# Performance work log

Measured on AMD Instinct MI355X. Metric: run time of the kernel, lower is better.

The kernel has to match this reference:

```python
import jax, jax.numpy as jnp
import numpy as np

D = 1024       # embedding_dim
H = 16         # num_attention_heads
B = 2
S = 2048       # seq_len == context_len


def setup_inputs() -> dict:
    key = jax.random.key(0)
    k1, k2, k3 = jax.random.split(key, 3)
    X = jax.random.normal(k1, (B, S, D), dtype=jnp.float32)
    W_qkv = jax.random.normal(k2, (D, 3 * D), dtype=jnp.float32) * 0.02
    b_qkv = jnp.zeros((3 * D,), dtype=jnp.float32)
    W_out = jax.random.normal(k3, (D, D), dtype=jnp.float32) * 0.02
    b_out = jnp.zeros((D,), dtype=jnp.float32)
    return {"X": X, "W_qkv": W_qkv, "b_qkv": b_qkv, "W_out": W_out, "b_out": b_out}


def reference(X, W_qkv, b_qkv, W_out, b_out):
    b, s, d = X.shape
    hd = d // H
    # fused QKV projection (GPT-2 Conv1D == x @ W + b)
    qkv = X @ W_qkv + b_qkv                       # [b, s, 3d]
    q, k, v = jnp.split(qkv, 3, axis=2)
    # [b, h, s, hd]
    q = q.reshape(b, s, H, hd).transpose(0, 2, 1, 3)
    k = k.reshape(b, s, H, hd).transpose(0, 2, 1, 3)
    v = v.reshape(b, s, H, hd).transpose(0, 2, 1, 3)
    # NOTE: source scales by rsqrt(embedding_dim), not head_dim
    scale = 1.0 / jnp.sqrt(jnp.float32(d))
    scores = jnp.einsum("bhqd,bhkd->bhqk", q, k) * scale
    causal = jnp.tril(jnp.ones((s, s), dtype=bool))
    scores = jnp.where(causal[None, None], scores, -jnp.inf)
    # attention_dropout applied pre-softmax in source; identity at eval (p used here = 0)
    probs = jax.nn.softmax(scores, axis=-1)
    attn = jnp.einsum("bhqk,bhkd->bhqd", probs, v)
    attn = attn.transpose(0, 2, 1, 3).reshape(b, s, d)
    out = attn @ W_out + b_out                    # outwards proj; dropout eval = identity
    return out
```

## Files before the change

### kernel.cpp

```cpp
#include <hip/hip_runtime.h>

#define S_LEN 2048
#define DIM   1024
#define NHEAD 16
#define HDIM  64
#define Q_PRESCALE 0.045084220027780106f

typedef __attribute__((ext_vector_type(8))) short  short8;
typedef __attribute__((ext_vector_type(4))) float  floatx4;
typedef __attribute__((ext_vector_type(4))) unsigned short ushort4v;

__device__ inline unsigned short f2bf(float f) {
  unsigned v = __builtin_bit_cast(unsigned, f);
  v += 0x7FFFu + ((v >> 16) & 1u);
  return (unsigned short)(v >> 16);
}

__device__ inline void async16(const unsigned short* g, unsigned short* l) {
  __builtin_amdgcn_global_load_lds(
      (const __attribute__((address_space(1))) unsigned int*)g,
      (__attribute__((address_space(3))) unsigned int*)l, 16, 0, 0);
}

__global__ __launch_bounds__(256) void prep_kernel(
    const float* __restrict__ X, const float* __restrict__ Wqkv,
    const float* __restrict__ Wout, unsigned short* __restrict__ Xb,
    unsigned short* __restrict__ Wqkvt, unsigned short* __restrict__ Woutt) {
  const int j = blockIdx.x, t = threadIdx.x;
  if (j >= 4096) {
    int i = ((j - 4096) * 256 + t) * 8;
    float4 a = *(const float4*)&X[i];
    float4 b = *(const float4*)&X[i + 4];
    short8 o;
    o[0] = (short)f2bf(a.x); o[1] = (short)f2bf(a.y);
    o[2] = (short)f2bf(a.z); o[3] = (short)f2bf(a.w);
    o[4] = (short)f2bf(b.x); o[5] = (short)f2bf(b.y);
    o[6] = (short)f2bf(b.z); o[7] = (short)f2bf(b.w);
    *(short8*)&Xb[i] = o;
    return;
  }
  __shared__ unsigned short tile[32][33];
  const float* in; unsigned short* out; int N, tn, tk;
  if (j < 3072) { in = Wqkv; out = Wqkvt; N = 3072; tn = j % 96; tk = j / 96; }
  else { int u = j - 3072; in = Wout; out = Woutt; N = 1024; tn = u & 31; tk = u >> 5; }
  const int n0 = tn * 32, k0 = tk * 32;
  const int tx = t & 31, ty = t >> 5;
#pragma unroll
  for (int i = 0; i < 32; i += 8)
    tile[ty + i][tx] = f2bf(in[(size_t)(k0 + ty + i) * N + n0 + tx]);
  __syncthreads();
#pragma unroll
  for (int i = 0; i < 32; i += 8)
    out[(size_t)(n0 + ty + i) * 1024 + k0 + tx] = tile[tx][ty + i];
}

#define GEMM128_BODY(APTR, BPTR)                                                   \
  __shared__ __align__(16) unsigned short As[128][64];                             \
  __shared__ __align__(16) unsigned short Bs[128][64];                             \
  const int m0 = blockIdx.y * 128, n0 = blockIdx.x * 128;                          \
  const int t = threadIdx.x, lane = t & 63, wave = t >> 6;                         \
  const int quad = lane >> 4, l16 = lane & 15;                                     \
  const int wm = (wave >> 1) * 64, wn = (wave & 1) * 64;                           \
  const int lr = lane >> 3, lc = lane & 7, sc8 = (lc ^ lr) * 8;                    \
  const int sw = l16 & 7;                                                          \
  const int pA0 = (quad ^ sw) * 8, pA1 = ((4 + quad) ^ sw) * 8;                    \
  floatx4 acc[4][4];                                                               \
  _Pragma("unroll") for (int mi = 0; mi < 4; mi++)                                 \
      _Pragma("unroll") for (int ni = 0; ni < 4; ni++)                             \
          acc[mi][ni] = (floatx4){0.f, 0.f, 0.f, 0.f};                             \
  for (int k0 = 0; k0 < DIM; k0 += 64) {                                           \
    _Pragma("unroll") for (int i = 0; i < 4; i++) {                                \
      int rb = wave * 32 + i * 8;                                                  \
      async16(&APTR[(size_t)(m0 + rb + lr) * DIM + k0 + sc8], &As[rb][0]);         \
      async16(&BPTR[(size_t)(n0 + rb + lr) * DIM + k0 + sc8], &Bs[rb][0]);         \
    }                                                                              \
    __syncthreads();                                                               \
    short8 a0[4], a1[4];                                                           \
    _Pragma("unroll") for (int mi = 0; mi < 4; mi++) {                             \
      int row = wm + mi * 16 + l16;                                                \
      a0[mi] = *(const short8*)&As[row][pA0];                                      \
      a1[mi] = *(const short8*)&As[row][pA1];                                      \
    }                                                                              \
    _Pragma("unroll") for (int ni = 0; ni < 4; ni++) {                             \
      int row = wn + ni * 16 + l16;                                                \
      short8 b0 = *(const short8*)&Bs[row][pA0];                                   \
      short8 b1 = *(const short8*)&Bs[row][pA1];                                   \
      _Pragma("unroll") for (int mi = 0; mi < 4; mi++) {                           \
        acc[mi][ni] = __builtin_amdgcn_mfma_f32_16x16x32_bf16(a0[mi], b0, acc[mi][ni], 0, 0, 0); \
        acc[mi][ni] = __builtin_amdgcn_mfma_f32_16x16x32_bf16(a1[mi], b1, acc[mi][ni], 0, 0, 0); \
      }                                                                            \
    }                                                                              \
    __syncthreads();                                                               \
  }

__global__ __launch_bounds__(256) void gemm_qkv128(
    const unsigned short* __restrict__ Xb,
    const unsigned short* __restrict__ Wt,
    const float* __restrict__ bias,
    unsigned short* __restrict__ Qg,
    unsigned short* __restrict__ Kg,
    unsigned short* __restrict__ Vgt) {
  GEMM128_BODY(Xb, Wt)
  const int section = n0 >> 10;
  const int head = ((n0 + wn) >> 6) & 15;
#pragma unroll
  for (int mi = 0; mi < 4; mi++) {
    int mg = m0 + wm + mi * 16 + quad * 4;
    int bb = mg >> 11, sb = mg & 2047;
    size_t y = (size_t)bb * NHEAD + head;
    if (section == 2) {
#pragma unroll
      for (int ni = 0; ni < 4; ni++) {
        int hdi = ni * 16 + l16;
        float bv = bias[n0 + wn + hdi];
        ushort4v o;
#pragma unroll
        for (int r = 0; r < 4; r++) o[r] = f2bf(acc[mi][ni][r] + bv);
        *(ushort4v*)&Vgt[(y * HDIM + hdi) * S_LEN + sb] = o;
      }
    } else if (section == 0) {
#pragma unroll
      for (int ni = 0; ni < 4; ni++) {
        int hdi = ni * 16 + l16;
        float bv = bias[n0 + wn + hdi];
#pragma unroll
        for (int r = 0; r < 4; r++)
          Qg[(y * S_LEN + sb + r) * HDIM + hdi] = f2bf((acc[mi][ni][r] + bv) * Q_PRESCALE);
      }
    } else {
#pragma unroll
      for (int ni = 0; ni < 4; ni++) {
        int hdi = ni * 16 + l16;
        float bv = bias[n0 + wn + hdi];
#pragma unroll
        for (int r = 0; r < 4; r++)
          Kg[(y * S_LEN + sb + r) * HDIM + hdi] = f2bf(acc[mi][ni][r] + bv);
      }
    }
  }
}

__global__ __launch_bounds__(256) void gemm_out128(
    const unsigned short* __restrict__ A,
    const unsigned short* __restrict__ Wt,
    const float* __restrict__ bias,
    float* __restrict__ outp) {
  GEMM128_BODY(A, Wt)
#pragma unroll
  for (int ni = 0; ni < 4; ni++) {
    int n = n0 + wn + ni * 16 + l16;
    float bv = bias[n];
#pragma unroll
    for (int mi = 0; mi < 4; mi++) {
      int mg = m0 + wm + mi * 16 + quad * 4;
#pragma unroll
      for (int r = 0; r < 4; r++)
        outp[(size_t)(mg + r) * DIM + n] = acc[mi][ni][r] + bv;
    }
  }
}

__global__ __launch_bounds__(256) void gemm_qkv_kernel(
    const float* __restrict__ X,
    const unsigned short* __restrict__ Wt,
    const float* __restrict__ bias,
    unsigned short* __restrict__ Qg,
    unsigned short* __restrict__ Kg,
    unsigned short* __restrict__ Vgt,
    int g0, int G) {
  __shared__ __align__(16) unsigned short As[64][72];
  __shared__ __align__(16) unsigned short Bs[64][72];
  const int tn = blockIdx.x;
  const int section = tn / G, within = tn % G;
  const int n0 = section * 1024 + (g0 + within) * 64;
  const int m0 = blockIdx.y * 64;
  const int t = threadIdx.x, lane = t & 63, wave = t >> 6;
  const int quad = lane >> 4, l16 = lane & 15;

  floatx4 acc[4];
#pragma unroll
  for (int i = 0; i < 4; i++) acc[i] = (floatx4){0.f, 0.f, 0.f, 0.f};

  for (int k0 = 0; k0 < DIM; k0 += 64) {
#pragma unroll
    for (int i = 0; i < 2; i++) {
      int v = t + i * 256;
      int row = v >> 3, cc = (v & 7) * 8;
      float4 f0 = *(const float4*)&X[(size_t)(m0 + row) * DIM + k0 + cc];
      float4 f1 = *(const float4*)&X[(size_t)(m0 + row) * DIM + k0 + cc + 4];
      short8 o;
      o[0] = (short)f2bf(f0.x); o[1] = (short)f2bf(f0.y);
      o[2] = (short)f2bf(f0.z); o[3] = (short)f2bf(f0.w);
      o[4] = (short)f2bf(f1.x); o[5] = (short)f2bf(f1.y);
      o[6] = (short)f2bf(f1.z); o[7] = (short)f2bf(f1.w);
      *(short8*)&As[row][cc] = o;
      *(short8*)&Bs[row][cc] = *(const short8*)&Wt[(size_t)(n0 + row) * DIM + k0 + cc];
    }
    __syncthreads();
    short8 a0 = *(const short8*)&As[wave * 16 + l16][quad * 8];
    short8 a1 = *(const short8*)&As[wave * 16 + l16][32 + quad * 8];
#pragma unroll
    for (int nt = 0; nt < 4; nt++) {
      short8 b0 = *(const short8*)&Bs[nt * 16 + l16][quad * 8];
      short8 b1 = *(const short8*)&Bs[nt * 16 + l16][32 + quad * 8];
      acc[nt] = __builtin_amdgcn_mfma_f32_16x16x32_bf16(a0, b0, acc[nt], 0, 0, 0);
      acc[nt] = __builtin_amdgcn_mfma_f32_16x16x32_bf16(a1, b1, acc[nt], 0, 0, 0);
    }
    __syncthreads();
  }

  const int mbase = m0 + wave * 16 + quad * 4;
  const int b = mbase >> 11, sbase = mbase & 2047;
  const int y = b * G + within;
  if (section == 2) {
#pragma unroll
    for (int nt = 0; nt < 4; nt++) {
      int hdi = nt * 16 + l16;
      float bv = bias[n0 + hdi];
      ushort4v o;
#pragma unroll
      for (int r = 0; r < 4; r++) o[r] = f2bf(acc[nt][r] + bv);
      *(ushort4v*)&Vgt[((size_t)y * HDIM + hdi) * S_LEN + sbase] = o;
    }
  } else if (section == 0) {
#pragma unroll
    for (int nt = 0; nt < 4; nt++) {
      int hdi = nt * 16 + l16;
      float bv = bias[n0 + hdi];
#pragma unroll
      for (int r = 0; r < 4; r++)
        Qg[((size_t)y * S_LEN + sbase + r) * HDIM + hdi] =
            f2bf((acc[nt][r] + bv) * Q_PRESCALE);
    }
  } else {
#pragma unroll
    for (int nt = 0; nt < 4; nt++) {
      int hdi = nt * 16 + l16;
      float bv = bias[n0 + hdi];
#pragma unroll
      for (int r = 0; r < 4; r++)
        Kg[((size_t)y * S_LEN + sbase + r) * HDIM + hdi] = f2bf(acc[nt][r] + bv);
    }
  }
}

__global__ __launch_bounds__(256) void attn_kernel(
    const unsigned short* __restrict__ Qg,
    const unsigned short* __restrict__ Kg,
    const unsigned short* __restrict__ Vgt,
    unsigned short* __restrict__ attnB) {
  __shared__ __align__(16) unsigned short Ks[2][64][64];
  __shared__ __align__(16) unsigned short Vs[2][64][64];
  __shared__ __align__(16) unsigned short Ones[16][64];
  __shared__ __align__(16) unsigned short Ps[4][16][72];

  const int y = blockIdx.x;
  const int b = y >> 4, h = y & 15;
  const int qt = 31 - blockIdx.y;
  const int q0 = qt * 64;
  const int nT = qt + 1;
  const int t = threadIdx.x;
  const int lane = t & 63, wave = t >> 6;
  const int quad = lane >> 4, l16 = lane & 15;
  const int lr = lane >> 3, lc = lane & 7;
  const int sc8 = (lc ^ lr) * 8;
  const int sw = l16 & 7;
  const int p0 = (quad ^ sw) * 8, p1 = ((4 + quad) ^ sw) * 8;

  const unsigned short* Qh = Qg + (size_t)y * S_LEN * HDIM;
  const unsigned short* Kh = Kg + (size_t)y * S_LEN * HDIM;
  const unsigned short* Vh = Vgt + (size_t)y * HDIM * S_LEN;

  if (t < 128) {
    int row = t >> 3, c = (t & 7) * 8;
    unsigned short vv = (row == 0) ? (unsigned short)0x3F80 : (unsigned short)0;
    short8 o;
#pragma unroll
    for (int j = 0; j < 8; j++) o[j] = (short)vv;
    *(short8*)&Ones[row][c] = o;
  }

  short8 aq0, aq1;
  {
    const unsigned short* qp = &Qh[(size_t)(q0 + wave * 16 + l16) * HDIM];
    aq0 = *(const short8*)&qp[quad * 8];
    aq1 = *(const short8*)&qp[32 + quad * 8];
  }

  floatx4 o_acc[5];
#pragma unroll
  for (int dt = 0; dt < 5; dt++) o_acc[dt] = (floatx4){0.f, 0.f, 0.f, 0.f};

  {
    int rb = wave * 16;
#pragma unroll
    for (int i = 0; i < 2; i++) {
      async16(&Kh[(size_t)(rb + i * 8 + lr) * HDIM + sc8], &Ks[0][rb + i * 8][0]);
      async16(&Vh[(size_t)(rb + i * 8 + lr) * S_LEN + sc8], &Vs[0][rb + i * 8][0]);
    }
  }

  for (int tt = 0; tt < nT; tt++) {
    const int j0 = tt * 64;
    const int buf = tt & 1;
    __syncthreads();
    if (tt + 1 < nT) {
      int j1 = j0 + 64, nb = 1 - buf;
      int rb = wave * 16;
#pragma unroll
      for (int i = 0; i < 2; i++) {
        async16(&Kh[(size_t)(j1 + rb + i * 8 + lr) * HDIM + sc8], &Ks[nb][rb + i * 8][0]);
        async16(&Vh[(size_t)(rb + i * 8 + lr) * S_LEN + j1 + sc8], &Vs[nb][rb + i * 8][0]);
      }
    }

    floatx4 sc[4];
#pragma unroll
    for (int nt = 0; nt < 4; nt++) {
      short8 kb0 = *(const short8*)&Ks[buf][nt * 16 + l16][p0];
      short8 kb1 = *(const short8*)&Ks[buf][nt * 16 + l16][p1];
      sc[nt] = (floatx4){0.f, 0.f, 0.f, 0.f};
      sc[nt] = __builtin_amdgcn_mfma_f32_16x16x32_bf16(aq0, kb0, sc[nt], 0, 0, 0);
      sc[nt] = __builtin_amdgcn_mfma_f32_16x16x32_bf16(aq1, kb1, sc[nt], 0, 0, 0);
    }

    if (j0 == q0) {
#pragma unroll
      for (int nt = 0; nt < 4; nt++) {
        int keyl = nt * 16 + l16;
#pragma unroll
        for (int r = 0; r < 4; r++) {
          int ql = wave * 16 + quad * 4 + r;
          float p = exp2f(sc[nt][r]);
          p = (keyl <= ql) ? p : 0.f;
          Ps[wave][quad * 4 + r][nt * 16 + l16] = f2bf(p);
        }
      }
    } else {
#pragma unroll
      for (int nt = 0; nt < 4; nt++)
#pragma unroll
        for (int r = 0; r < 4; r++)
          Ps[wave][quad * 4 + r][nt * 16 + l16] = f2bf(exp2f(sc[nt][r]));
    }
    short8 ap0 = *(const short8*)&Ps[wave][l16][quad * 8];
    short8 ap1 = *(const short8*)&Ps[wave][l16][32 + quad * 8];

#pragma unroll
    for (int dt = 0; dt < 5; dt++) {
      short8 vb0 = (dt < 4) ? *(const short8*)&Vs[buf][dt * 16 + l16][p0]
                            : *(const short8*)&Ones[l16][p0];
      short8 vb1 = (dt < 4) ? *(const short8*)&Vs[buf][dt * 16 + l16][p1]
                            : *(const short8*)&Ones[l16][p1];
      o_acc[dt] = __builtin_amdgcn_mfma_f32_16x16x32_bf16(ap0, vb0, o_acc[dt], 0, 0, 0);
      o_acc[dt] = __builtin_amdgcn_mfma_f32_16x16x32_bf16(ap1, vb1, o_acc[dt], 0, 0, 0);
    }
  }

  float linv[4];
#pragma unroll
  for (int r = 0; r < 4; r++)
    linv[r] = 1.0f / __shfl(o_acc[4][r], quad << 4);
#pragma unroll
  for (int dt = 0; dt < 4; dt++)
#pragma unroll
    for (int r = 0; r < 4; r++) {
      int qg = q0 + wave * 16 + quad * 4 + r;
      attnB[(size_t)(b * S_LEN + qg) * DIM + h * HDIM + dt * 16 + l16] =
          f2bf(o_acc[dt][r] * linv[r]);
    }
}

extern "C" void kernel_launch(void* const* d_in, const int* in_sizes, int n_in,
                              void* d_out, int out_size, void* d_ws, size_t ws_size,
                              hipStream_t stream) {
  const float* X    = (const float*)d_in[0];
  const float* Wqkv = (const float*)d_in[1];
  const float* bqkv = (const float*)d_in[2];
  const float* Wout = (const float*)d_in[3];
  const float* bout = (const float*)d_in[4];
  float* outp = (float*)d_out;

  unsigned short* Wqkvt = (unsigned short*)d_ws;
  unsigned short* Woutt = Wqkvt + (size_t)3145728;
  unsigned short* attnB = Woutt + (size_t)1048576;
  unsigned short* Qg    = attnB + (size_t)4194304;
  unsigned short* Kg    = Qg + (size_t)4194304;
  unsigned short* Vgt   = Kg + (size_t)4194304;
  unsigned short* Xb    = Vgt + (size_t)4194304;

  const bool bigWs = ws_size >= (size_t)48 * 1024 * 1024;

  if (bigWs) {
    prep_kernel<<<6144, 256, 0, stream>>>(X, Wqkv, Wout, Xb, Wqkvt, Woutt);
    gemm_qkv128<<<dim3(24, 32), 256, 0, stream>>>(Xb, Wqkvt, bqkv, Qg, Kg, Vgt);
  } else {
    prep_kernel<<<4096, 256, 0, stream>>>(X, Wqkv, Wout, nullptr, Wqkvt, Woutt);
    gemm_qkv_kernel<<<dim3(48, 64), 256, 0, stream>>>(
        X, Wqkvt, bqkv, Qg, Kg, Vgt, 0, 16);
  }
  attn_kernel<<<dim3(32, 32), 256, 0, stream>>>(Qg, Kg, Vgt, attnB);
  gemm_out128<<<dim3(8, 32), 256, 0, stream>>>(attnB, Woutt, bout, outp);
}
```

Baseline: 190.9 us.

## Keep attention probabilities in registers via transposed QK MFMA and lane shuffles

The QK^T MFMA operands are swapped so each lane holds scores in a transposed layout. The probabilities are then packed to bf16 with v_cvt_pk_bf16_f32 and redistributed across lanes with shuffles into the A-operand layout for the PV MFMA. This removes the per-tile round trip through the shared-memory P buffer and the shared Ones buffer. The cost is many ds_bpermute shuffles and selects per tile, and the hardware cvt rounding may differ slightly from the manual rounding.

New measurement: 191.4 us. About the same (+0.3%).

```diff
diff --git a/kernel.cpp b/kernel.cpp
--- a/kernel.cpp
+++ b/kernel.cpp
@@ -9,11 +9,18 @@
 typedef __attribute__((ext_vector_type(8))) short  short8;
 typedef __attribute__((ext_vector_type(4))) float  floatx4;
 typedef __attribute__((ext_vector_type(4))) unsigned short ushort4v;
+typedef __attribute__((ext_vector_type(4))) unsigned int uintx4;
 
 __device__ inline unsigned short f2bf(float f) {
   unsigned v = __builtin_bit_cast(unsigned, f);
   v += 0x7FFFu + ((v >> 16) & 1u);
   return (unsigned short)(v >> 16);
+}
+
+__device__ inline unsigned cvt_pk_bf16(float a, float b) {
+  unsigned r;
+  asm("v_cvt_pk_bf16_f32 %0, %1, %2" : "=v"(r) : "v"(a), "v"(b));
+  return r;
 }
 
 __device__ inline void async16(const unsigned short* g, unsigned short* l) {
@@ -251,8 +258,6 @@
     unsigned short* __restrict__ attnB) {
   __shared__ __align__(16) unsigned short Ks[2][64][64];
   __shared__ __align__(16) unsigned short Vs[2][64][64];
-  __shared__ __align__(16) unsigned short Ones[16][64];
-  __shared__ __align__(16) unsigned short Ps[4][16][72];
 
   const int y = blockIdx.x;
   const int b = y >> 4, h = y & 15;
@@ -271,14 +276,13 @@
   const unsigned short* Kh = Kg + (size_t)y * S_LEN * HDIM;
   const unsigned short* Vh = Vgt + (size_t)y * HDIM * S_LEN;
 
-  if (t < 128) {
-    int row = t >> 3, c = (t & 7) * 8;
-    unsigned short vv = (row == 0) ? (unsigned short)0x3F80 : (unsigned short)0;
-    short8 o;
-#pragma unroll
-    for (int j = 0; j < 8; j++) o[j] = (short)vv;
-    *(short8*)&Ones[row][c] = o;
-  }
+  const unsigned ov = (l16 == 0) ? 0x3F803F80u : 0u;
+  const uintx4 ou = {ov, ov, ov, ov};
+  const short8 ones = __builtin_bit_cast(short8, ou);
+
+  const int srcA = (((2 * quad) & 3) << 4) | l16;
+  const int srcB = (((2 * quad + 1) & 3) << 4) | l16;
+  const bool hiq = (quad & 2) != 0;
 
   short8 aq0, aq1;
   {
@@ -320,38 +324,48 @@
       short8 kb0 = *(const short8*)&Ks[buf][nt * 16 + l16][p0];
       short8 kb1 = *(const short8*)&Ks[buf][nt * 16 + l16][p1];
       sc[nt] = (floatx4){0.f, 0.f, 0.f, 0.f};
-      sc[nt] = __builtin_amdgcn_mfma_f32_16x16x32_bf16(aq0, kb0, sc[nt], 0, 0, 0);
-      sc[nt] = __builtin_amdgcn_mfma_f32_16x16x32_bf16(aq1, kb1, sc[nt], 0, 0, 0);
-    }
-
+      sc[nt] = __builtin_amdgcn_mfma_f32_16x16x32_bf16(kb0, aq0, sc[nt], 0, 0, 0);
+      sc[nt] = __builtin_amdgcn_mfma_f32_16x16x32_bf16(kb1, aq1, sc[nt], 0, 0, 0);
+    }
+
+    float p[4][4];
+#pragma unroll
+    for (int nt = 0; nt < 4; nt++)
+#pragma unroll
+      for (int r = 0; r < 4; r++)
+        p[nt][r] = exp2f(sc[nt][r]);
     if (j0 == q0) {
-#pragma unroll
-      for (int nt = 0; nt < 4; nt++) {
-        int keyl = nt * 16 + l16;
-#pragma unroll
-        for (int r = 0; r < 4; r++) {
-          int ql = wave * 16 + quad * 4 + r;
-          float p = exp2f(sc[nt][r]);
-          p = (keyl <= ql) ? p : 0.f;
-          Ps[wave][quad * 4 + r][nt * 16 + l16] = f2bf(p);
-        }
-      }
-    } else {
+      const int ql = wave * 16 + l16;
 #pragma unroll
       for (int nt = 0; nt < 4; nt++)
 #pragma unroll
         for (int r = 0; r < 4; r++)
-          Ps[wave][quad * 4 + r][nt * 16 + l16] = f2bf(exp2f(sc[nt][r]));
-    }
-    short8 ap0 = *(const short8*)&Ps[wave][l16][quad * 8];
-    short8 ap1 = *(const short8*)&Ps[wave][l16][32 + quad * 8];
+          if (nt * 16 + quad * 4 + r > ql) p[nt][r] = 0.f;
+    }
+
+    unsigned pk00 = cvt_pk_bf16(p[0][0], p[0][1]), pk01 = cvt_pk_bf16(p[0][2], p[0][3]);
+    unsigned pk10 = cvt_pk_bf16(p[1][0], p[1][1]), pk11 = cvt_pk_bf16(p[1][2], p[1][3]);
+    unsigned pk20 = cvt_pk_bf16(p[2][0], p[2][1]), pk21 = cvt_pk_bf16(p[2][2], p[2][3]);
+    unsigned pk30 = cvt_pk_bf16(p[3][0], p[3][1]), pk31 = cvt_pk_bf16(p[3][2], p[3][3]);
+
+    unsigned w0a = __shfl(pk00, srcA), w0b = __shfl(pk10, srcA);
+    unsigned w1a = __shfl(pk01, srcA), w1b = __shfl(pk11, srcA);
+    unsigned w2a = __shfl(pk00, srcB), w2b = __shfl(pk10, srcB);
+    unsigned w3a = __shfl(pk01, srcB), w3b = __shfl(pk11, srcB);
+    uintx4 u0 = {hiq ? w0b : w0a, hiq ? w1b : w1a, hiq ? w2b : w2a, hiq ? w3b : w3a};
+    short8 ap0 = __builtin_bit_cast(short8, u0);
+
+    unsigned w4a = __shfl(pk20, srcA), w4b = __shfl(pk30, srcA);
+    unsigned w5a = __shfl(pk21, srcA), w5b = __shfl(pk31, srcA);
+    unsigned w6a = __shfl(pk20, srcB), w6b = __shfl(pk30, srcB);
+    unsigned w7a = __shfl(pk21, srcB), w7b = __shfl(pk31, srcB);
+    uintx4 u1 = {hiq ? w4b : w4a, hiq ? w5b : w5a, hiq ? w6b : w6a, hiq ? w7b : w7a};
+    short8 ap1 = __builtin_bit_cast(short8, u1);
 
 #pragma unroll
     for (int dt = 0; dt < 5; dt++) {
-      short8 vb0 = (dt < 4) ? *(const short8*)&Vs[buf][dt * 16 + l16][p0]
-                            : *(const short8*)&Ones[l16][p0];
-      short8 vb1 = (dt < 4) ? *(const short8*)&Vs[buf][dt * 16 + l16][p1]
-                            : *(const short8*)&Ones[l16][p1];
+      short8 vb0 = (dt < 4) ? *(const short8*)&Vs[buf][dt * 16 + l16][p0] : ones;
+      short8 vb1 = (dt < 4) ? *(const short8*)&Vs[buf][dt * 16 + l16][p1] : ones;
       o_acc[dt] = __builtin_amdgcn_mfma_f32_16x16x32_bf16(ap0, vb0, o_acc[dt], 0, 0, 0);
       o_acc[dt] = __builtin_amdgcn_mfma_f32_16x16x32_bf16(ap1, vb1, o_acc[dt], 0, 0, 0);
     }
```

## Rewrite attention with 32x32 MFMA, 128-query tiles and register-resident P

Applied to the files above, without the earlier changes.

The attention kernel moves from 16x16x32 to 32x32x16 bf16 MFMA, with each wave owning 32 queries, so each block covers 128 queries and the grid in y is halved. The score tile is computed transposed (K as the A operand), which lets P be packed to bf16 and rearranged with permlane32_swap instead of a round trip through shared memory. The row-sum-by-ones trick now uses a register constant rather than an LDS array. This removes LDS traffic and a sync point for P and raises MFMA efficiency, but the larger tiles leave fewer blocks and add more causal-diagonal masking work per block.

New measurement: 204.1 us. +6.9%, slower.

```diff
diff --git a/kernel.cpp b/kernel.cpp
--- a/kernel.cpp
+++ b/kernel.cpp
@@ -8,12 +8,20 @@
 
 typedef __attribute__((ext_vector_type(8))) short  short8;
 typedef __attribute__((ext_vector_type(4))) float  floatx4;
+typedef __attribute__((ext_vector_type(16))) float floatx16;
 typedef __attribute__((ext_vector_type(4))) unsigned short ushort4v;
+typedef __attribute__((ext_vector_type(4))) unsigned int uintx4;
 
 __device__ inline unsigned short f2bf(float f) {
   unsigned v = __builtin_bit_cast(unsigned, f);
   v += 0x7FFFu + ((v >> 16) & 1u);
   return (unsigned short)(v >> 16);
+}
+
+__device__ inline unsigned cvt_pk_bf16(float a, float b) {
+  unsigned r;
+  asm("v_cvt_pk_bf16_f32 %0, %1, %2" : "=v"(r) : "v"(a), "v"(b));
+  return r;
 }
 
 __device__ inline void async16(const unsigned short* g, unsigned short* l) {
@@ -251,45 +259,36 @@
     unsigned short* __restrict__ attnB) {
   __shared__ __align__(16) unsigned short Ks[2][64][64];
   __shared__ __align__(16) unsigned short Vs[2][64][64];
-  __shared__ __align__(16) unsigned short Ones[16][64];
-  __shared__ __align__(16) unsigned short Ps[4][16][72];
 
   const int y = blockIdx.x;
   const int b = y >> 4, h = y & 15;
-  const int qt = 31 - blockIdx.y;
-  const int q0 = qt * 64;
-  const int nT = qt + 1;
+  const int qt = 15 - blockIdx.y;
+  const int q0 = qt * 128;
+  const int nT = 2 * (qt + 1);
   const int t = threadIdx.x;
   const int lane = t & 63, wave = t >> 6;
-  const int quad = lane >> 4, l16 = lane & 15;
+  const int l31 = lane & 31, g = lane >> 5, l7 = lane & 7;
   const int lr = lane >> 3, lc = lane & 7;
   const int sc8 = (lc ^ lr) * 8;
-  const int sw = l16 & 7;
-  const int p0 = (quad ^ sw) * 8, p1 = ((4 + quad) ^ sw) * 8;
 
   const unsigned short* Qh = Qg + (size_t)y * S_LEN * HDIM;
   const unsigned short* Kh = Kg + (size_t)y * S_LEN * HDIM;
   const unsigned short* Vh = Vgt + (size_t)y * HDIM * S_LEN;
 
-  if (t < 128) {
-    int row = t >> 3, c = (t & 7) * 8;
-    unsigned short vv = (row == 0) ? (unsigned short)0x3F80 : (unsigned short)0;
-    short8 o;
-#pragma unroll
-    for (int j = 0; j < 8; j++) o[j] = (short)vv;
-    *(short8*)&Ones[row][c] = o;
-  }
-
-  short8 aq0, aq1;
+  const unsigned ov = (l31 == 0) ? 0x3F803F80u : 0u;
+  const uintx4 ou = {ov, ov, ov, ov};
+  const short8 ones = __builtin_bit_cast(short8, ou);
+
+  short8 bq[4];
   {
-    const unsigned short* qp = &Qh[(size_t)(q0 + wave * 16 + l16) * HDIM];
-    aq0 = *(const short8*)&qp[quad * 8];
-    aq1 = *(const short8*)&qp[32 + quad * 8];
-  }
-
-  floatx4 o_acc[5];
-#pragma unroll
-  for (int dt = 0; dt < 5; dt++) o_acc[dt] = (floatx4){0.f, 0.f, 0.f, 0.f};
+    const unsigned short* qp = &Qh[(size_t)(q0 + wave * 32 + l31) * HDIM + g * 8];
+#pragma unroll
+    for (int ks = 0; ks < 4; ks++) bq[ks] = *(const short8*)&qp[ks * 16];
+  }
+
+  floatx16 oa0, oa1, osum;
+#pragma unroll
+  for (int i = 0; i < 16; i++) { oa0[i] = 0.f; oa1[i] = 0.f; osum[i] = 0.f; }
 
   {
     int rb = wave * 16;
@@ -305,7 +304,7 @@
     const int buf = tt & 1;
     __syncthreads();
     if (tt + 1 < nT) {
-      int j1 = j0 + 64, nb = 1 - buf;
+      int j1 = j0 + 64, nb = buf ^ 1;
       int rb = wave * 16;
 #pragma unroll
       for (int i = 0; i < 2; i++) {
@@ -314,61 +313,78 @@
       }
     }
 
-    floatx4 sc[4];
-#pragma unroll
-    for (int nt = 0; nt < 4; nt++) {
-      short8 kb0 = *(const short8*)&Ks[buf][nt * 16 + l16][p0];
-      short8 kb1 = *(const short8*)&Ks[buf][nt * 16 + l16][p1];
-      sc[nt] = (floatx4){0.f, 0.f, 0.f, 0.f};
-      sc[nt] = __builtin_amdgcn_mfma_f32_16x16x32_bf16(aq0, kb0, sc[nt], 0, 0, 0);
-      sc[nt] = __builtin_amdgcn_mfma_f32_16x16x32_bf16(aq1, kb1, sc[nt], 0, 0, 0);
-    }
-
-    if (j0 == q0) {
-#pragma unroll
-      for (int nt = 0; nt < 4; nt++) {
-        int keyl = nt * 16 + l16;
-#pragma unroll
-        for (int r = 0; r < 4; r++) {
-          int ql = wave * 16 + quad * 4 + r;
-          float p = exp2f(sc[nt][r]);
-          p = (keyl <= ql) ? p : 0.f;
-          Ps[wave][quad * 4 + r][nt * 16 + l16] = f2bf(p);
-        }
+    floatx16 s0, s1;
+#pragma unroll
+    for (int i = 0; i < 16; i++) { s0[i] = 0.f; s1[i] = 0.f; }
+#pragma unroll
+    for (int ks = 0; ks < 4; ks++) {
+      short8 ak0 = *(const short8*)&Ks[buf][l31][((2 * ks + g) ^ l7) * 8];
+      s0 = __builtin_amdgcn_mfma_f32_32x32x16_bf16(ak0, bq[ks], s0, 0, 0, 0);
+    }
+#pragma unroll
+    for (int ks = 0; ks < 4; ks++) {
+      short8 ak1 = *(const short8*)&Ks[buf][32 + l31][((2 * ks + g) ^ l7) * 8];
+      s1 = __builtin_amdgcn_mfma_f32_32x32x16_bf16(ak1, bq[ks], s1, 0, 0, 0);
+    }
+
+    float p0a[16], p1a[16];
+#pragma unroll
+    for (int r = 0; r < 16; r++) {
+      p0a[r] = exp2f(s0[r]);
+      p1a[r] = exp2f(s1[r]);
+    }
+    if (tt >= nT - 2) {
+      const int qv = q0 + wave * 32 + l31;
+#pragma unroll
+      for (int r = 0; r < 16; r++) {
+        const int off = (r & 3) + 8 * (r >> 2) + 4 * g;
+        if (j0 + off > qv) p0a[r] = 0.f;
+        if (j0 + 32 + off > qv) p1a[r] = 0.f;
       }
-    } else {
-#pragma unroll
-      for (int nt = 0; nt < 4; nt++)
-#pragma unroll
-        for (int r = 0; r < 4; r++)
-          Ps[wave][quad * 4 + r][nt * 16 + l16] = f2bf(exp2f(sc[nt][r]));
-    }
-    short8 ap0 = *(const short8*)&Ps[wave][l16][quad * 8];
-    short8 ap1 = *(const short8*)&Ps[wave][l16][32 + quad * 8];
-
-#pragma unroll
-    for (int dt = 0; dt < 5; dt++) {
-      short8 vb0 = (dt < 4) ? *(const short8*)&Vs[buf][dt * 16 + l16][p0]
-                            : *(const short8*)&Ones[l16][p0];
-      short8 vb1 = (dt < 4) ? *(const short8*)&Vs[buf][dt * 16 + l16][p1]
-                            : *(const short8*)&Ones[l16][p1];
-      o_acc[dt] = __builtin_amdgcn_mfma_f32_16x16x32_bf16(ap0, vb0, o_acc[dt], 0, 0, 0);
-      o_acc[dt] = __builtin_amdgcn_mfma_f32_16x16x32_bf16(ap1, vb1, o_acc[dt], 0, 0, 0);
-    }
-  }
-
-  float linv[4];
-#pragma unroll
-  for (int r = 0; r < 4; r++)
-    linv[r] = 1.0f / __shfl(o_acc[4][r], quad << 4);
-#pragma unroll
-  for (int dt = 0; dt < 4; dt++)
-#pragma unroll
-    for (int r = 0; r < 4; r++) {
-      int qg = q0 + wave * 16 + quad * 4 + r;
-      attnB[(size_t)(b * S_LEN + qg) * DIM + h * HDIM + dt * 16 + l16] =
-          f2bf(o_acc[dt][r] * linv[r]);
-    }
+    }
+
+    unsigned pk0[8], pk1[8];
+#pragma unroll
+    for (int m = 0; m < 8; m++) {
+      pk0[m] = cvt_pk_bf16(p0a[2 * m], p0a[2 * m + 1]);
+      pk1[m] = cvt_pk_bf16(p1a[2 * m], p1a[2 * m + 1]);
+    }
+
+    short8 ap[4];
+#pragma unroll
+    for (int sh = 0; sh < 2; sh++) {
+      auto r0 = __builtin_amdgcn_permlane32_swap(pk0[4 * sh + 0], pk0[4 * sh + 2], false, false);
+      auto r1 = __builtin_amdgcn_permlane32_swap(pk0[4 * sh + 1], pk0[4 * sh + 3], false, false);
+      uintx4 u0 = {(unsigned)r0[0], (unsigned)r1[0], (unsigned)r0[1], (unsigned)r1[1]};
+      ap[sh] = __builtin_bit_cast(short8, u0);
+      auto r2 = __builtin_amdgcn_permlane32_swap(pk1[4 * sh + 0], pk1[4 * sh + 2], false, false);
+      auto r3 = __builtin_amdgcn_permlane32_swap(pk1[4 * sh + 1], pk1[4 * sh + 3], false, false);
+      uintx4 u1 = {(unsigned)r2[0], (unsigned)r3[0], (unsigned)r2[1], (unsigned)r3[1]};
+      ap[2 + sh] = __builtin_bit_cast(short8, u1);
+    }
+
+#pragma unroll
+    for (int ks = 0; ks < 4; ks++) {
+      short8 bv0 = *(const short8*)&Vs[buf][l31][((2 * ks + g) ^ l7) * 8];
+      oa0 = __builtin_amdgcn_mfma_f32_32x32x16_bf16(ap[ks], bv0, oa0, 0, 0, 0);
+      short8 bv1 = *(const short8*)&Vs[buf][32 + l31][((2 * ks + g) ^ l7) * 8];
+      oa1 = __builtin_amdgcn_mfma_f32_32x32x16_bf16(ap[ks], bv1, oa1, 0, 0, 0);
+      osum = __builtin_amdgcn_mfma_f32_32x32x16_bf16(ap[ks], ones, osum, 0, 0, 0);
+    }
+  }
+
+  float linv[16];
+#pragma unroll
+  for (int r = 0; r < 16; r++)
+    linv[r] = 1.0f / __shfl(osum[r], lane & 32);
+
+#pragma unroll
+  for (int r = 0; r < 16; r++) {
+    int qgl = q0 + wave * 32 + (r & 3) + 8 * (r >> 2) + 4 * g;
+    size_t base = (size_t)(b * S_LEN + qgl) * DIM + h * HDIM;
+    attnB[base + l31]      = f2bf(oa0[r] * linv[r]);
+    attnB[base + 32 + l31] = f2bf(oa1[r] * linv[r]);
+  }
 }
 
 extern "C" void kernel_launch(void* const* d_in, const int* in_sizes, int n_in,
@@ -399,6 +415,6 @@
     gemm_qkv_kernel<<<dim3(48, 64), 256, 0, stream>>>(
         X, Wqkvt, bqkv, Qg, Kg, Vgt, 0, 16);
   }
-  attn_kernel<<<dim3(32, 32), 256, 0, stream>>>(Qg, Kg, Vgt, attnB);
+  attn_kernel<<<dim3(32, 16), 256, 0, stream>>>(Qg, Kg, Vgt, attnB);
   gemm_out128<<<dim3(8, 32), 256, 0, stream>>>(attnB, Woutt, bout, outp);
 }
```
